# Optimization experiments

Measured on AMD Instinct MI355X. Metric: run time of the kernel, lower is better.

Reference implementation:

```python
import jax, jax.numpy as jnp
import numpy as np

B, N, HID = 8192, 64, 512  # batch, spatial dim n, hidden width


def setup_inputs() -> dict:
    key = jax.random.key(0)
    ks = jax.random.split(key, 6)
    d = 3 * N
    return {
        "x": jax.random.normal(ks[0], (B, N), jnp.float32),
        "q": jax.random.normal(ks[1], (B, N), jnp.float32),
        "p": jax.random.normal(ks[2], (B, N), jnp.float32),
        "W1": jax.random.normal(ks[3], (d, HID), jnp.float32) / np.float32(np.sqrt(d)),
        "b1": jnp.zeros((HID,), jnp.float32),
        "W2": jax.random.normal(ks[4], (HID, HID), jnp.float32) / np.float32(np.sqrt(HID)),
        "b2": jnp.zeros((HID,), jnp.float32),
        "W3": jax.random.normal(ks[5], (HID, 1), jnp.float32) / np.float32(np.sqrt(HID)),
        "b3": jnp.zeros((1,), jnp.float32),
    }


def reference(x, q, p, W1, b1, W2, b2, W3, b3):
    """Returns (q_dot_hat, p_dot_hat) = (-dH_dp_dx, -dH_dq_dx), each [B, N].

    Faithful to HNN1DWaveSeparable.forward: the torch code takes, per column j,
    d/dx_j of (dH/dq)_j and (dH/dp)_j -- i.e. the diagonals of the mixed Hessian
    blocks H_{q,x} and H_{p,x}. Computed here in one fused per-sample Hessian
    (the torch version redundantly re-runs H and loops torch.autograd.grad).
    """
    n = x.shape[1]

    def H(z):  # z: [3n] -> scalar Hamiltonian
        h = jnp.tanh(z @ W1 + b1)
        h = jnp.tanh(h @ W2 + b2)
        return (h @ W3 + b3)[0]

    def per_sample(xs, qs, ps):
        z = jnp.concatenate([xs, qs, ps])          # [3n]
        hess = jax.hessian(H)(z)                   # [3n, 3n]
        dH_dq_dx = jnp.diagonal(hess[n:2 * n, :n])  # d2H/(dq_j dx_j)
        dH_dp_dx = jnp.diagonal(hess[2 * n:, :n])   # d2H/(dp_j dx_j)
        return -dH_dp_dx, -dH_dq_dx

    return jax.vmap(per_sample)(x, q, p)
```

## Files before the change

kernel.cpp:

```cpp
#include <hip/hip_runtime.h>

#define BATCH 8192
#define NQ 64
#define HID 512
#define DIN 192
#define NT 512
#define SPB1 16
#define SPB2 32
#define SPB 2

typedef _Float16 f16;
typedef _Float16 f16x8 __attribute__((ext_vector_type(8)));
typedef _Float16 f16x4 __attribute__((ext_vector_type(4)));
typedef float f32x4 __attribute__((ext_vector_type(4)));

__device__ f16 g_w2fragT[HID * HID];
__device__ f16 g_w2fragR[HID * HID];
__device__ f16   g_h1[(size_t)BATCH * HID];
__device__ float g_t1[(size_t)BATCH * HID];
__device__ float g_n2h1t1[(size_t)BATCH * HID];
__device__ float g_c[(size_t)BATCH * HID];
__device__ float g_s[(size_t)BATCH * HID];

__global__ void prep_frag(const float* __restrict__ W2) {
    const int k = blockIdx.x;
    const int m = threadIdx.x;
    const f16 v = (f16)W2[k * HID + m];
    g_w2fragT[(size_t)((((m >> 4) * 16 + (k >> 5)) * 64) + ((m & 15) | (((k >> 3) & 3) << 4))) * 8 + (k & 7)] = v;
    g_w2fragR[(size_t)((((k >> 4) * 16 + (m >> 5)) * 64) + ((k & 15) | (((m >> 3) & 3) << 4))) * 8 + (m & 7)] = v;
}

__global__ __launch_bounds__(NT)
void fwd1(const float* __restrict__ x, const float* __restrict__ q,
          const float* __restrict__ p, const float* __restrict__ W1,
          const float* __restrict__ b1) {
    __shared__ float zs[SPB1][DIN];
    const int b0 = blockIdx.x * SPB1;
    const int tid = threadIdx.x;
    for (int i = tid; i < SPB1 * DIN; i += NT) {
        const int s = i / DIN, kk = i % DIN;
        float v;
        if (kk < NQ)          v = x[(b0 + s) * NQ + kk];
        else if (kk < 2 * NQ) v = q[(b0 + s) * NQ + kk - NQ];
        else                  v = p[(b0 + s) * NQ + kk - 2 * NQ];
        zs[s][kk] = v;
    }
    __syncthreads();
    const int m = tid;
    float acc[SPB1];
    #pragma unroll
    for (int s = 0; s < SPB1; ++s) acc[s] = 0.f;
    #pragma unroll 2
    for (int k = 0; k < DIN; ++k) {
        const float w = W1[k * HID + m];
        #pragma unroll
        for (int s = 0; s < SPB1; ++s) acc[s] += zs[s][k] * w;
    }
    const float bb = b1[m];
    #pragma unroll
    for (int s = 0; s < SPB1; ++s) {
        const float h1 = tanhf(acc[s] + bb);
        const float t1 = 1.f - h1 * h1;
        const size_t idx = (size_t)(b0 + s) * HID + m;
        g_h1[idx] = (f16)h1;
        g_t1[idx] = t1;
        g_n2h1t1[idx] = -2.f * h1 * t1;
    }
}

__global__ __launch_bounds__(NT)
void fwd23(const float* __restrict__ b2, const float* __restrict__ W3) {
    __shared__ f16 alds[SPB2 * HID];
    const int b0 = blockIdx.x * SPB2;
    const int tid = threadIdx.x, lane = tid & 63, wv = tid >> 6;
    const int l15 = lane & 15, qd = lane >> 4;
    const int n0 = wv * 64;

    {
        const int s = tid >> 4;
        f16x8* a8 = (f16x8*)alds;
        #pragma unroll
        for (int c = 0; c < 4; ++c) {
            const int kc = (tid & 15) + c * 16;
            const f16x8 v = *(const f16x8*)&g_h1[(size_t)(b0 + s) * HID + kc * 8];
            a8[s * 64 + (kc ^ (s & 7))] = v;
        }
    }
    __syncthreads();

    const f16x8* a8 = (const f16x8*)alds;
    auto aload = [&](f16x8* AF, int kn) {
        #pragma unroll
        for (int jt = 0; jt < 2; ++jt) {
            const int row = jt * 16 + l15;
            AF[jt] = a8[row * 64 + ((kn * 4 + qd) ^ (row & 7))];
        }
    };
    auto bloadT = [&](f16x8* BF, int kn) {
        #pragma unroll
        for (int nt = 0; nt < 4; ++nt)
            BF[nt] = *(const f16x8*)&g_w2fragT[(size_t)((((wv * 4 + nt) * 16 + kn) * 64) + lane) * 8];
    };
    auto bloadR = [&](f16x8* BF, int kn) {
        #pragma unroll
        for (int nt = 0; nt < 4; ++nt)
            BF[nt] = *(const f16x8*)&g_w2fragR[(size_t)((((wv * 4 + nt) * 16 + kn) * 64) + lane) * 8];
    };

    f32x4 acc[2][4];
    #pragma unroll
    for (int a = 0; a < 2; ++a)
        #pragma unroll
        for (int c = 0; c < 4; ++c) acc[a][c] = (f32x4){0.f, 0.f, 0.f, 0.f};
    auto cluster = [&](const f16x8* AF, const f16x8* BF) {
        #pragma unroll
        for (int jt = 0; jt < 2; ++jt)
            #pragma unroll
            for (int nt = 0; nt < 4; ++nt)
                acc[jt][nt] = __builtin_amdgcn_mfma_f32_16x16x32_f16(AF[jt], BF[nt], acc[jt][nt], 0, 0, 0);
    };

    {
        f16x8 aA[2], bA[4], aB[2], bB[4];
        aload(aA, 0); bloadT(bA, 0);
        #pragma unroll 1
        for (int ks = 0; ks < 16; ks += 2) {
            aload(aB, ks + 1); bloadT(bB, ks + 1);
            cluster(aA, bA);
            if (ks + 2 < 16) { aload(aA, ks + 2); bloadT(bA, ks + 2); }
            cluster(aB, bB);
        }
    }

    float v2v[2][4][4];
    #pragma unroll
    for (int nt = 0; nt < 4; ++nt) {
        const int mcol = n0 + nt * 16 + l15;
        const float bb = b2[mcol], w3 = W3[mcol];
        #pragma unroll
        for (int jt = 0; jt < 2; ++jt) {
            #pragma unroll
            for (int r = 0; r < 4; ++r) {
                const int srow = jt * 16 + qd * 4 + r;
                const float h2 = tanhf(acc[jt][nt][r] + bb);
                const float t2 = 1.f - h2 * h2;
                const float v2 = w3 * t2;
                v2v[jt][nt][r] = v2;
                g_c[(size_t)(b0 + srow) * HID + mcol] = -2.f * h2 * v2;
            }
        }
    }
    __syncthreads();

    #pragma unroll
    for (int nt = 0; nt < 4; ++nt) {
        const int mcol = n0 + nt * 16 + l15;
        #pragma unroll
        for (int jt = 0; jt < 2; ++jt) {
            #pragma unroll
            for (int r = 0; r < 4; ++r) {
                const int srow = jt * 16 + qd * 4 + r;
                alds[srow * HID + (((mcol >> 3) ^ (srow & 7)) << 3) + (mcol & 7)] = (f16)v2v[jt][nt][r];
            }
        }
    }
    __syncthreads();

    #pragma unroll
    for (int a = 0; a < 2; ++a)
        #pragma unroll
        for (int c = 0; c < 4; ++c) acc[a][c] = (f32x4){0.f, 0.f, 0.f, 0.f};
    {
        f16x8 aA[2], bA[4], aB[2], bB[4];
        aload(aA, 0); bloadR(bA, 0);
        #pragma unroll 1
        for (int ms = 0; ms < 16; ms += 2) {
            aload(aB, ms + 1); bloadR(bB, ms + 1);
            cluster(aA, bA);
            if (ms + 2 < 16) { aload(aA, ms + 2); bloadR(bA, ms + 2); }
            cluster(aB, bB);
        }
    }

    #pragma unroll
    for (int nt = 0; nt < 4; ++nt) {
        const int kcol = n0 + nt * 16 + l15;
        #pragma unroll
        for (int jt = 0; jt < 2; ++jt) {
            #pragma unroll
            for (int r = 0; r < 4; ++r) {
                const int srow = jt * 16 + qd * 4 + r;
                const size_t idx = (size_t)(b0 + srow) * HID + kcol;
                g_s[idx] = g_n2h1t1[idx] * acc[jt][nt][r];
            }
        }
    }
}

__global__ __launch_bounds__(NT, 2)
void hnn_main(const float* __restrict__ W1, float* __restrict__ out) {
    __shared__ f16 awF[SPB][NQ * HID];
    __shared__ float t1s[SPB][HID], cs[SPB][HID], ss[SPB][HID];
    __shared__ float red[SPB][8][NQ][2];

    const int tid = threadIdx.x, lane = tid & 63, wv = tid >> 6;
    const int l15 = lane & 15, qd = lane >> 4;
    const int b0 = blockIdx.x * SPB;

    #pragma unroll
    for (int s = 0; s < SPB; ++s) {
        t1s[s][tid] = g_t1[(size_t)(b0 + s) * HID + tid];
        cs[s][tid]  = g_c[(size_t)(b0 + s) * HID + tid];
        ss[s][tid]  = g_s[(size_t)(b0 + s) * HID + tid];
    }

    {
        const int col0 = lane * 8;
        const float4 ta0 = *(const float4*)&g_t1[(size_t)(b0 + 0) * HID + col0];
        const float4 tb0 = *(const float4*)&g_t1[(size_t)(b0 + 0) * HID + col0 + 4];
        const float4 ta1 = *(const float4*)&g_t1[(size_t)(b0 + 1) * HID + col0];
        const float4 tb1 = *(const float4*)&g_t1[(size_t)(b0 + 1) * HID + col0 + 4];
        f16x8* aw80 = (f16x8*)awF[0];
        f16x8* aw81 = (f16x8*)awF[1];
        #pragma unroll
        for (int jr = 0; jr < 8; ++jr) {
            const int j = wv * 8 + jr;
            const float4 wa = *(const float4*)&W1[(size_t)j * HID + col0];
            const float4 wb = *(const float4*)&W1[(size_t)j * HID + col0 + 4];
            f16x8 h0, h1v;
            h0[0] = (f16)(wa.x * ta0.x); h0[1] = (f16)(wa.y * ta0.y);
            h0[2] = (f16)(wa.z * ta0.z); h0[3] = (f16)(wa.w * ta0.w);
            h0[4] = (f16)(wb.x * tb0.x); h0[5] = (f16)(wb.y * tb0.y);
            h0[6] = (f16)(wb.z * tb0.z); h0[7] = (f16)(wb.w * tb0.w);
            h1v[0] = (f16)(wa.x * ta1.x); h1v[1] = (f16)(wa.y * ta1.y);
            h1v[2] = (f16)(wa.z * ta1.z); h1v[3] = (f16)(wa.w * ta1.w);
            h1v[4] = (f16)(wb.x * tb1.x); h1v[5] = (f16)(wb.y * tb1.y);
            h1v[6] = (f16)(wb.z * tb1.z); h1v[7] = (f16)(wb.w * tb1.w);
            aw80[j * 64 + (lane ^ (j & 7))] = h0;
            aw81[j * 64 + (lane ^ (j & 7))] = h1v;
        }
    }
    __syncthreads();

    const int n0 = wv * 64;
    f32x4 acc4[SPB][4][4];
    #pragma unroll
    for (int s = 0; s < SPB; ++s)
        #pragma unroll
        for (int a = 0; a < 4; ++a)
            #pragma unroll
            for (int c = 0; c < 4; ++c) acc4[s][a][c] = (f32x4){0.f, 0.f, 0.f, 0.f};

    auto xloadS = [&](f16x8* XF, int kn, int s) {
        const f16x8* a8 = (const f16x8*)awF[s];
        #pragma unroll
        for (int jt = 0; jt < 4; ++jt) {
            const int row = jt * 16 + l15;
            XF[jt] = a8[row * 64 + ((kn * 4 + qd) ^ (row & 7))];
        }
    };
    auto wloadT = [&](f16x8* WF, int kn) {
        #pragma unroll
        for (int nt = 0; nt < 4; ++nt)
            WF[nt] = *(const f16x8*)&g_w2fragT[(size_t)((((wv * 4 + nt) * 16 + kn) * 64) + lane) * 8];
    };
    auto wloadR = [&](f16x8* WF, int kn) {
        #pragma unroll
        for (int nt = 0; nt < 4; ++nt)
            WF[nt] = *(const f16x8*)&g_w2fragR[(size_t)((((wv * 4 + nt) * 16 + kn) * 64) + lane) * 8];
    };
    auto clusterE = [&](const f16x8* WF, const f16x8* XF, int s) {
        #pragma unroll
        for (int mt = 0; mt < 4; ++mt)
            #pragma unroll
            for (int jt = 0; jt < 4; ++jt)
                acc4[s][mt][jt] = __builtin_amdgcn_mfma_f32_16x16x32_f16(WF[mt], XF[jt], acc4[s][mt][jt], 0, 0, 0);
    };
    auto clusterR = [&](const f16x8* XF, const f16x8* WF, int s) {
        #pragma unroll
        for (int jt = 0; jt < 4; ++jt)
            #pragma unroll
            for (int nt = 0; nt < 4; ++nt)
                acc4[s][jt][nt] = __builtin_amdgcn_mfma_f32_16x16x32_f16(XF[jt], WF[nt], acc4[s][jt][nt], 0, 0, 0);
    };

    {
        f16x8 xP[4], xQ[4], wA[4], wB[4];
        xloadS(xP, 0, 0); wloadT(wA, 0);
        #pragma unroll 1
        for (int ks = 0; ks < 16; ks += 2) {
            xloadS(xQ, ks, 1);
            wloadT(wB, ks + 1);
            clusterE(wA, xP, 0);
            xloadS(xP, ks + 1, 0);
            clusterE(wA, xQ, 1);
            xloadS(xQ, ks + 1, 1);
            if (ks + 2 < 16) wloadT(wA, ks + 2);
            clusterE(wB, xP, 0);
            if (ks + 2 < 16) xloadS(xP, ks + 2, 0);
            clusterE(wB, xQ, 1);
        }
    }
    __syncthreads();

    #pragma unroll
    for (int s = 0; s < SPB; ++s) {
        #pragma unroll
        for (int mt = 0; mt < 4; ++mt) {
            const int mbase = n0 + mt * 16 + qd * 4;
            const float4 cv = *(const float4*)&cs[s][mbase];
            const int chunk = mbase >> 3;
            const int half4 = (mbase >> 2) & 1;
            #pragma unroll
            for (int jt = 0; jt < 4; ++jt) {
                const int j = jt * 16 + l15;
                f16x4 h;
                h[0] = (f16)(acc4[s][mt][jt][0] * cv.x);
                h[1] = (f16)(acc4[s][mt][jt][1] * cv.y);
                h[2] = (f16)(acc4[s][mt][jt][2] * cv.z);
                h[3] = (f16)(acc4[s][mt][jt][3] * cv.w);
                *(f16x4*)&awF[s][j * HID + ((chunk ^ (j & 7)) << 3) + half4 * 4] = h;
            }
        }
    }
    __syncthreads();

    #pragma unroll
    for (int s = 0; s < SPB; ++s)
        #pragma unroll
        for (int a = 0; a < 4; ++a)
            #pragma unroll
            for (int c = 0; c < 4; ++c) acc4[s][a][c] = (f32x4){0.f, 0.f, 0.f, 0.f};
    {
        f16x8 xP[4], xQ[4], wA[4], wB[4];
        xloadS(xP, 0, 0); wloadR(wA, 0);
        #pragma unroll 1
        for (int ms = 0; ms < 16; ms += 2) {
            xloadS(xQ, ms, 1);
            wloadR(wB, ms + 1);
            clusterR(xP, wA, 0);
            xloadS(xP, ms + 1, 0);
            clusterR(xQ, wA, 1);
            xloadS(xQ, ms + 1, 1);
            if (ms + 2 < 16) wloadR(wA, ms + 2);
            clusterR(xP, wB, 0);
            if (ms + 2 < 16) xloadS(xP, ms + 2, 0);
            clusterR(xQ, wB, 1);
        }
    }

    float t1k[SPB][4], sk[SPB][4];
    #pragma unroll
    for (int s = 0; s < SPB; ++s)
        #pragma unroll
        for (int nt = 0; nt < 4; ++nt) {
            const int k = n0 + nt * 16 + l15;
            t1k[s][nt] = t1s[s][k];
            sk[s][nt]  = ss[s][k];
        }
    #pragma unroll
    for (int jt = 0; jt < 4; ++jt) {
        #pragma unroll
        for (int r = 0; r < 4; ++r) {
            const int j = jt * 16 + qd * 4 + r;
            float vq0 = 0.f, vp0 = 0.f, vq1 = 0.f, vp1 = 0.f;
            #pragma unroll
            for (int nt = 0; nt < 4; ++nt) {
                const int k = n0 + nt * 16 + l15;
                const float w1x = W1[(size_t)j * HID + k];
                const float w1q = W1[(size_t)(NQ + j) * HID + k];
                const float w1p = W1[(size_t)(2 * NQ + j) * HID + k];
                const float base0 = acc4[0][jt][nt][r] * t1k[0][nt] + sk[0][nt] * w1x;
                const float base1 = acc4[1][jt][nt][r] * t1k[1][nt] + sk[1][nt] * w1x;
                vq0 += w1q * base0; vp0 += w1p * base0;
                vq1 += w1q * base1; vp1 += w1p * base1;
            }
            vq0 += __shfl_xor(vq0, 1, 64); vq0 += __shfl_xor(vq0, 2, 64);
            vq0 += __shfl_xor(vq0, 4, 64); vq0 += __shfl_xor(vq0, 8, 64);
            vp0 += __shfl_xor(vp0, 1, 64); vp0 += __shfl_xor(vp0, 2, 64);
            vp0 += __shfl_xor(vp0, 4, 64); vp0 += __shfl_xor(vp0, 8, 64);
            vq1 += __shfl_xor(vq1, 1, 64); vq1 += __shfl_xor(vq1, 2, 64);
            vq1 += __shfl_xor(vq1, 4, 64); vq1 += __shfl_xor(vq1, 8, 64);
            vp1 += __shfl_xor(vp1, 1, 64); vp1 += __shfl_xor(vp1, 2, 64);
            vp1 += __shfl_xor(vp1, 4, 64); vp1 += __shfl_xor(vp1, 8, 64);
            if (l15 == 0) {
                red[0][wv][j][0] = vq0;
                red[0][wv][j][1] = vp0;
                red[1][wv][j][0] = vq1;
                red[1][wv][j][1] = vp1;
            }
        }
    }
    __syncthreads();

    if (tid < SPB * NQ * 2) {
        const int s = tid >> 7, j = (tid >> 1) & 63, c = tid & 1;
        float v = 0.f;
        #pragma unroll
        for (int w = 0; w < 8; ++w) v += red[s][w][j][c];
        if (c == 0) out[(size_t)BATCH * NQ + (size_t)(b0 + s) * NQ + j] = -v;
        else        out[(size_t)(b0 + s) * NQ + j] = -v;
    }
}

extern "C" void kernel_launch(void* const* d_in, const int* in_sizes, int n_in,
                              void* d_out, int out_size, void* d_ws, size_t ws_size,
                              hipStream_t stream) {
    const float* x  = (const float*)d_in[0];
    const float* q  = (const float*)d_in[1];
    const float* p  = (const float*)d_in[2];
    const float* W1 = (const float*)d_in[3];
    const float* b1 = (const float*)d_in[4];
    const float* W2 = (const float*)d_in[5];
    const float* b2 = (const float*)d_in[6];
    const float* W3 = (const float*)d_in[7];
    float* out = (float*)d_out;

    prep_frag<<<HID, HID, 0, stream>>>(W2);
    fwd1<<<BATCH / SPB1, NT, 0, stream>>>(x, q, p, W1, b1);
    fwd23<<<BATCH / SPB2, NT, 0, stream>>>(b2, W3);
    hnn_main<<<BATCH / SPB, NT, 0, stream>>>(W1, out);
}
```

Measured before the change: 636.3 us.

## Factor the s*W1x term into a precomputed G-matrix MFMA GEMM

The s_k*W1x[j,k]*W1q/p[j,k] term is split out of the per-sample reduction in hnn_main. It becomes a batched GEMM of s against a precomputed 128x512 matrix G = W1q∘W1x / W1p∘W1x, stored in f16 MFMA fragment layout. A new fwd4 kernel computes this term into g_t2, and hnn_main adds it during the final reduction. This removes one W1 load, the ss shared array and FMAs from the hot loop, at the cost of an extra kernel launch, an f16 rounding of s and G, and extra global traffic.

After: 627.7 us. No clear change (-1.3%).

```diff
diff --git a/kernel.cpp b/kernel.cpp
--- a/kernel.cpp
+++ b/kernel.cpp
@@ -16,11 +16,13 @@
 
 __device__ f16 g_w2fragT[HID * HID];
 __device__ f16 g_w2fragR[HID * HID];
+__device__ f16 g_Gfrag[128 * HID];
 __device__ f16   g_h1[(size_t)BATCH * HID];
 __device__ float g_t1[(size_t)BATCH * HID];
 __device__ float g_n2h1t1[(size_t)BATCH * HID];
 __device__ float g_c[(size_t)BATCH * HID];
 __device__ float g_s[(size_t)BATCH * HID];
+__device__ float g_t2[(size_t)BATCH * 128];
 
 __global__ void prep_frag(const float* __restrict__ W2) {
     const int k = blockIdx.x;
@@ -28,6 +30,16 @@
     const f16 v = (f16)W2[k * HID + m];
     g_w2fragT[(size_t)((((m >> 4) * 16 + (k >> 5)) * 64) + ((m & 15) | (((k >> 3) & 3) << 4))) * 8 + (k & 7)] = v;
     g_w2fragR[(size_t)((((k >> 4) * 16 + (m >> 5)) * 64) + ((k & 15) | (((m >> 3) & 3) << 4))) * 8 + (m & 7)] = v;
+}
+
+__global__ void prep_g(const float* __restrict__ W1) {
+    const int j = blockIdx.x;
+    const int k = threadIdx.x;
+    const int jj = j & 63;
+    const float w = (j < 64)
+        ? W1[(64 + jj) * HID + k] * W1[jj * HID + k]
+        : W1[(128 + jj) * HID + k] * W1[jj * HID + k];
+    g_Gfrag[(size_t)((((j >> 4) * 16 + (k >> 5)) * 64) + ((j & 15) | (((k >> 3) & 3) << 4))) * 8 + (k & 7)] = (f16)w;
 }
 
 __global__ __launch_bounds__(NT)
@@ -197,10 +209,57 @@
     }
 }
 
+__global__ __launch_bounds__(NT)
+void fwd4() {
+    __shared__ f16 alds[SPB2 * HID];
+    const int b0 = blockIdx.x * SPB2;
+    const int tid = threadIdx.x, lane = tid & 63, wv = tid >> 6;
+    const int l15 = lane & 15, qd = lane >> 4;
+    {
+        const int sr = tid >> 4;
+        f16x8* a8 = (f16x8*)alds;
+        #pragma unroll
+        for (int c = 0; c < 4; ++c) {
+            const int kc = (tid & 15) + c * 16;
+            const float* sp = &g_s[(size_t)(b0 + sr) * HID + kc * 8];
+            f16x8 h;
+            #pragma unroll
+            for (int e = 0; e < 8; ++e) h[e] = (f16)sp[e];
+            a8[sr * 64 + (kc ^ (sr & 7))] = h;
+        }
+    }
+    __syncthreads();
+    f32x4 acc[2];
+    acc[0] = (f32x4){0.f, 0.f, 0.f, 0.f};
+    acc[1] = (f32x4){0.f, 0.f, 0.f, 0.f};
+    const f16x8* a8 = (const f16x8*)alds;
+    #pragma unroll 2
+    for (int ks = 0; ks < 16; ++ks) {
+        f16x8 afr[2], bfr;
+        #pragma unroll
+        for (int jt = 0; jt < 2; ++jt) {
+            const int row = jt * 16 + l15;
+            afr[jt] = a8[row * 64 + ((ks * 4 + qd) ^ (row & 7))];
+        }
+        bfr = *(const f16x8*)&g_Gfrag[(size_t)(((wv * 16 + ks) * 64) + lane) * 8];
+        #pragma unroll
+        for (int jt = 0; jt < 2; ++jt)
+            acc[jt] = __builtin_amdgcn_mfma_f32_16x16x32_f16(afr[jt], bfr, acc[jt], 0, 0, 0);
+    }
+    const int jc = wv * 16 + l15;
+    #pragma unroll
+    for (int jt = 0; jt < 2; ++jt)
+        #pragma unroll
+        for (int r = 0; r < 4; ++r) {
+            const int srow = jt * 16 + qd * 4 + r;
+            g_t2[(size_t)(b0 + srow) * 128 + jc] = acc[jt][r];
+        }
+}
+
 __global__ __launch_bounds__(NT, 2)
 void hnn_main(const float* __restrict__ W1, float* __restrict__ out) {
     __shared__ f16 awF[SPB][NQ * HID];
-    __shared__ float t1s[SPB][HID], cs[SPB][HID], ss[SPB][HID];
+    __shared__ float t1s[SPB][HID], cs[SPB][HID];
     __shared__ float red[SPB][8][NQ][2];
 
     const int tid = threadIdx.x, lane = tid & 63, wv = tid >> 6;
@@ -211,7 +270,6 @@
     for (int s = 0; s < SPB; ++s) {
         t1s[s][tid] = g_t1[(size_t)(b0 + s) * HID + tid];
         cs[s][tid]  = g_c[(size_t)(b0 + s) * HID + tid];
-        ss[s][tid]  = g_s[(size_t)(b0 + s) * HID + tid];
     }
 
     {
@@ -349,15 +407,12 @@
         }
     }
 
-    float t1k[SPB][4], sk[SPB][4];
+    float t1k[SPB][4];
     #pragma unroll
     for (int s = 0; s < SPB; ++s)
         #pragma unroll
-        for (int nt = 0; nt < 4; ++nt) {
-            const int k = n0 + nt * 16 + l15;
-            t1k[s][nt] = t1s[s][k];
-            sk[s][nt]  = ss[s][k];
-        }
+        for (int nt = 0; nt < 4; ++nt)
+            t1k[s][nt] = t1s[s][n0 + nt * 16 + l15];
     #pragma unroll
     for (int jt = 0; jt < 4; ++jt) {
         #pragma unroll
@@ -367,11 +422,10 @@
             #pragma unroll
             for (int nt = 0; nt < 4; ++nt) {
                 const int k = n0 + nt * 16 + l15;
-                const float w1x = W1[(size_t)j * HID + k];
                 const float w1q = W1[(size_t)(NQ + j) * HID + k];
                 const float w1p = W1[(size_t)(2 * NQ + j) * HID + k];
-                const float base0 = acc4[0][jt][nt][r] * t1k[0][nt] + sk[0][nt] * w1x;
-                const float base1 = acc4[1][jt][nt][r] * t1k[1][nt] + sk[1][nt] * w1x;
+                const float base0 = acc4[0][jt][nt][r] * t1k[0][nt];
+                const float base1 = acc4[1][jt][nt][r] * t1k[1][nt];
                 vq0 += w1q * base0; vp0 += w1p * base0;
                 vq1 += w1q * base1; vp1 += w1p * base1;
             }
@@ -398,6 +452,7 @@
         float v = 0.f;
         #pragma unroll
         for (int w = 0; w < 8; ++w) v += red[s][w][j][c];
+        v += g_t2[(size_t)(b0 + s) * 128 + c * 64 + j];
         if (c == 0) out[(size_t)BATCH * NQ + (size_t)(b0 + s) * NQ + j] = -v;
         else        out[(size_t)(b0 + s) * NQ + j] = -v;
     }
@@ -417,7 +472,9 @@
     float* out = (float*)d_out;
 
     prep_frag<<<HID, HID, 0, stream>>>(W2);
+    prep_g<<<128, HID, 0, stream>>>(W1);
     fwd1<<<BATCH / SPB1, NT, 0, stream>>>(x, q, p, W1, b1);
     fwd23<<<BATCH / SPB2, NT, 0, stream>>>(b2, W3);
+    fwd4<<<BATCH / SPB2, NT, 0, stream>>>();
     hnn_main<<<BATCH / SPB, NT, 0, stream>>>(W1, out);
 }
```
